# Kernel optimization log

Hardware: AMD Instinct MI355X
Metric: run time of the kernel (lower is better)

Reference implementation:

```python
import jax, jax.numpy as jnp
import numpy as np

N, M, D = 16384, 2048, 512


def setup_inputs() -> dict:
    key = jax.random.key(0)
    k1, k2 = jax.random.split(key)
    x = jax.random.normal(k1, (N, D), dtype=jnp.float32)
    centers = jax.random.normal(k2, (M, D), dtype=jnp.float32)
    log_sigmas = jnp.zeros((M,), dtype=jnp.float32)
    return {"x": x, "centers": centers, "log_sigmas": log_sigmas}


def reference(x, centers, log_sigmas):
    x_sq = jnp.sum(x * x, axis=1, keepdims=True)          # [N, 1]
    c_sq = jnp.sum(centers * centers, axis=1)             # [M]
    cross = jnp.einsum("nd,md->nm", x, centers)           # [N, M] GEMM
    d = x_sq + c_sq[None, :] - 2.0 * cross                # [N, M]
    sigmas = jnp.exp(log_sigmas)                          # [M]
    return jnp.exp(-d / (2.0 * sigmas[None, :] ** 2))     # [N, M]
```

## Files before the change

kernel.cpp:

```cpp
#include <hip/hip_runtime.h>
#include <hip/hip_bf16.h>
#include <stdint.h>

#define N_ROWS 16384
#define M_COLS 2048
#define D_DIM  512

typedef __attribute__((ext_vector_type(4))) float f32x4;
typedef __attribute__((ext_vector_type(2))) int   i32x2;
typedef long i64;

#define AS1 __attribute__((address_space(1)))
#define AS3 __attribute__((address_space(3)))

__global__ __launch_bounds__(256) void conv_all(const float* __restrict__ x,
                                                const float* __restrict__ cen,
                                                const float* __restrict__ ls,
                                                unsigned char* __restrict__ xb,
                                                unsigned char* __restrict__ cb,
                                                float* __restrict__ xsq,
                                                float* __restrict__ csq,
                                                float* __restrict__ nsc) {
  const int gr   = blockIdx.x * 4 + (threadIdx.x >> 6);
  const int lane = threadIdx.x & 63;
  const float* src;
  unsigned char* dst;
  float* sq;
  int row;
  bool is_c = (gr >= N_ROWS);
  if (is_c) { row = gr - N_ROWS; src = cen; dst = cb; sq = csq; }
  else      { row = gr;          src = x;   dst = xb; sq = xsq; }

  const float* s = src + (size_t)row * D_DIM + lane * 8;
  f32x4 v0 = *(const f32x4*)s;
  f32x4 v1 = *(const f32x4*)(s + 4);
  float acc = v0.x*v0.x + v0.y*v0.y + v0.z*v0.z + v0.w*v0.w
            + v1.x*v1.x + v1.y*v1.y + v1.z*v1.z + v1.w*v1.w;
  i32x2 o;
  int w0 = __builtin_amdgcn_cvt_pk_fp8_f32(v0.x, v0.y, 0, false);
  w0     = __builtin_amdgcn_cvt_pk_fp8_f32(v0.z, v0.w, w0, true);
  int w1 = __builtin_amdgcn_cvt_pk_fp8_f32(v1.x, v1.y, 0, false);
  w1     = __builtin_amdgcn_cvt_pk_fp8_f32(v1.z, v1.w, w1, true);
  o[0] = w0; o[1] = w1;
  *(i32x2*)(dst + (size_t)row * D_DIM + lane * 8) = o;
  #pragma unroll
  for (int off = 32; off > 0; off >>= 1) acc += __shfl_down(acc, off, 64);
  if (lane == 0) sq[row] = acc;
  if (is_c && lane == 1) nsc[row] = -0.5f * expf(-2.0f * ls[row]);
}

static __device__ __forceinline__ void gl2lds16(const unsigned char* g, unsigned char* l) {
  __builtin_amdgcn_global_load_lds((const AS1 uint32_t*)g, (AS3 uint32_t*)l, 16, 0, 0);
}

__global__ __launch_bounds__(256) void gemm_rbf(const unsigned char* __restrict__ A8,
                                                const unsigned char* __restrict__ B8,
                                                const float* __restrict__ xsq,
                                                const float* __restrict__ csq,
                                                const float* __restrict__ nscale,
                                                float* __restrict__ out) {
  __shared__ unsigned char As[128 * 128];
  __shared__ unsigned char Bs[128 * 128];

  const int t    = threadIdx.x;
  const int lane = t & 63;
  const int w    = t >> 6;
  const int wr   = w >> 1, wc = w & 1;
  const int rowBase = blockIdx.y * 128;
  const int colBase = blockIdx.x * 128;

  const int lrow = t >> 3;
  const int lkc  = ((t & 7) ^ ((t >> 3) & 7)) * 16;

  const unsigned char* aG = A8 + (size_t)(rowBase + lrow) * D_DIM + lkc;
  const unsigned char* bG = B8 + (size_t)(colBase + lrow) * D_DIM + lkc;
  unsigned char* aL = &As[t * 16];
  unsigned char* bL = &Bs[t * 16];

  f32x4 acc[4][4];
  #pragma unroll
  for (int i = 0; i < 4; ++i)
    #pragma unroll
    for (int j = 0; j < 4; ++j)
      #pragma unroll
      for (int r = 0; r < 4; ++r) acc[i][j][r] = 0.0f;

  const int fr  = lane & 15;
  const int q16 = lane >> 4;
  const int sw  = fr & 7;
  const int sub = (q16 & 1) * 8;

  for (int kt = 0; kt < D_DIM; kt += 128) {
    __syncthreads();
    #pragma unroll
    for (int q = 0; q < 4; ++q) {
      gl2lds16(aG + kt + (size_t)(q * 32) * D_DIM, aL + q * 4096);
      gl2lds16(bG + kt + (size_t)(q * 32) * D_DIM, bL + q * 4096);
    }
    __syncthreads();

    #pragma unroll
    for (int ks = 0; ks < 4; ++ks) {
      const int pc = ((ks * 2 + (q16 >> 1)) ^ sw) * 16 + sub;
      i64 af[4], bfr[4];
      #pragma unroll
      for (int i = 0; i < 4; ++i)
        af[i] = *(const i64*)&As[(wr * 64 + i * 16 + fr) * 128 + pc];
      #pragma unroll
      for (int j = 0; j < 4; ++j)
        bfr[j] = *(const i64*)&Bs[(wc * 64 + j * 16 + fr) * 128 + pc];

      #pragma unroll
      for (int i = 0; i < 4; ++i)
        #pragma unroll
        for (int j = 0; j < 4; ++j)
          acc[i][j] = __builtin_amdgcn_mfma_f32_16x16x32_fp8_fp8(af[i], bfr[j], acc[i][j], 0, 0, 0);
    }
  }

  const int rq = q16 * 4;
  float xs[4][4];
  #pragma unroll
  for (int i = 0; i < 4; ++i)
    #pragma unroll
    for (int r = 0; r < 4; ++r)
      xs[i][r] = xsq[rowBase + wr * 64 + i * 16 + rq + r];

  #pragma unroll
  for (int j = 0; j < 4; ++j) {
    const int c    = colBase + wc * 64 + j * 16 + fr;
    const float cs  = csq[c];
    const float nsc = nscale[c];
    #pragma unroll
    for (int i = 0; i < 4; ++i) {
      const int r0 = rowBase + wr * 64 + i * 16 + rq;
      #pragma unroll
      for (int r = 0; r < 4; ++r) {
        const float dv = xs[i][r] + cs - 2.0f * acc[i][j][r];
        out[(size_t)(r0 + r) * M_COLS + c] = __expf(dv * nsc);
      }
    }
  }
}

__global__ __launch_bounds__(256) void rbf_fallback(const float* __restrict__ x,
                                                    const float* __restrict__ cen,
                                                    const float* __restrict__ ls,
                                                    float* __restrict__ out) {
  __shared__ float xr[D_DIM];
  const int n = blockIdx.y;
  const int m = blockIdx.x * 256 + threadIdx.x;
  for (int d = threadIdx.x; d < D_DIM; d += 256) xr[d] = x[(size_t)n * D_DIM + d];
  __syncthreads();
  const float* cp = cen + (size_t)m * D_DIM;
  float acc = 0.f;
  for (int d = 0; d < D_DIM; d += 4) {
    f32x4 cv = *(const f32x4*)(cp + d);
    float d0 = xr[d + 0] - cv.x;
    float d1 = xr[d + 1] - cv.y;
    float d2 = xr[d + 2] - cv.z;
    float d3 = xr[d + 3] - cv.w;
    acc += d0 * d0 + d1 * d1 + d2 * d2 + d3 * d3;
  }
  const float nsc = -0.5f * expf(-2.0f * ls[m]);
  out[(size_t)n * M_COLS + m] = __expf(acc * nsc);
}

extern "C" void kernel_launch(void* const* d_in, const int* in_sizes, int n_in,
                              void* d_out, int out_size, void* d_ws, size_t ws_size,
                              hipStream_t stream) {
  const float* x   = (const float*)d_in[0];
  const float* cen = (const float*)d_in[1];
  const float* ls  = (const float*)d_in[2];
  float* out = (float*)d_out;

  const size_t need = (size_t)N_ROWS * D_DIM
                    + (size_t)M_COLS * D_DIM
                    + (size_t)N_ROWS * 4
                    + (size_t)M_COLS * 4
                    + (size_t)M_COLS * 4;

  if (ws_size >= need) {
    char* p = (char*)d_ws;
    unsigned char* xb = (unsigned char*)p; p += (size_t)N_ROWS * D_DIM;
    unsigned char* cb = (unsigned char*)p; p += (size_t)M_COLS * D_DIM;
    float* xsq   = (float*)p; p += (size_t)N_ROWS * 4;
    float* csq   = (float*)p; p += (size_t)M_COLS * 4;
    float* nsc   = (float*)p;

    conv_all<<<(N_ROWS + M_COLS) / 4, 256, 0, stream>>>(x, cen, ls, xb, cb, xsq, csq, nsc);
    dim3 grid(M_COLS / 128, N_ROWS / 128);
    gemm_rbf<<<grid, 256, 0, stream>>>(xb, cb, xsq, csq, nsc, out);
  } else {
    dim3 grid(M_COLS / 256, N_ROWS);
    rbf_fallback<<<grid, 256, 0, stream>>>(x, cen, ls, out);
  }
}
```

Measured before the change: 177.2 us.

## Load GEMM fragments directly from global memory into registers with prefetch

Drops the LDS staging and both barriers in the fp8 GEMM. Each lane now loads its MFMA operand fragments straight from global memory as 8-byte loads, double-buffered in registers with one k-step of prefetch. This removes shared-memory traffic and block synchronisation. In exchange, each wave re-reads operands from global/L2 with no cross-wave sharing, and the 8-byte strided loads are poorly coalesced, which likely raises memory traffic.

```diff
diff --git a/kernel.cpp b/kernel.cpp
--- a/kernel.cpp
+++ b/kernel.cpp
@@ -9,9 +9,6 @@
 typedef __attribute__((ext_vector_type(4))) float f32x4;
 typedef __attribute__((ext_vector_type(2))) int   i32x2;
 typedef long i64;
-
-#define AS1 __attribute__((address_space(1)))
-#define AS3 __attribute__((address_space(3)))
 
 __global__ __launch_bounds__(256) void conv_all(const float* __restrict__ x,
                                                 const float* __restrict__ cen,
@@ -49,19 +46,12 @@
   if (is_c && lane == 1) nsc[row] = -0.5f * expf(-2.0f * ls[row]);
 }
 
-static __device__ __forceinline__ void gl2lds16(const unsigned char* g, unsigned char* l) {
-  __builtin_amdgcn_global_load_lds((const AS1 uint32_t*)g, (AS3 uint32_t*)l, 16, 0, 0);
-}
-
 __global__ __launch_bounds__(256) void gemm_rbf(const unsigned char* __restrict__ A8,
                                                 const unsigned char* __restrict__ B8,
                                                 const float* __restrict__ xsq,
                                                 const float* __restrict__ csq,
                                                 const float* __restrict__ nscale,
                                                 float* __restrict__ out) {
-  __shared__ unsigned char As[128 * 128];
-  __shared__ unsigned char Bs[128 * 128];
-
   const int t    = threadIdx.x;
   const int lane = t & 63;
   const int w    = t >> 6;
@@ -69,13 +59,11 @@
   const int rowBase = blockIdx.y * 128;
   const int colBase = blockIdx.x * 128;
 
-  const int lrow = t >> 3;
-  const int lkc  = ((t & 7) ^ ((t >> 3) & 7)) * 16;
+  const int fr  = lane & 15;
+  const int q16 = lane >> 4;
 
-  const unsigned char* aG = A8 + (size_t)(rowBase + lrow) * D_DIM + lkc;
-  const unsigned char* bG = B8 + (size_t)(colBase + lrow) * D_DIM + lkc;
-  unsigned char* aL = &As[t * 16];
-  unsigned char* bL = &Bs[t * 16];
+  const unsigned char* aBase = A8 + (size_t)(rowBase + wr * 64 + fr) * D_DIM + q16 * 8;
+  const unsigned char* bBase = B8 + (size_t)(colBase + wc * 64 + fr) * D_DIM + q16 * 8;
 
   f32x4 acc[4][4];
   #pragma unroll
@@ -85,37 +73,30 @@
       #pragma unroll
       for (int r = 0; r < 4; ++r) acc[i][j][r] = 0.0f;
 
-  const int fr  = lane & 15;
-  const int q16 = lane >> 4;
-  const int sw  = fr & 7;
-  const int sub = (q16 & 1) * 8;
+  i64 aCur[4], bCur[4], aNxt[4], bNxt[4];
+  #pragma unroll
+  for (int i = 0; i < 4; ++i) {
+    aCur[i] = *(const i64*)(aBase + (size_t)(i * 16) * D_DIM);
+    bCur[i] = *(const i64*)(bBase + (size_t)(i * 16) * D_DIM);
+  }
 
-  for (int kt = 0; kt < D_DIM; kt += 128) {
-    __syncthreads();
+  #pragma unroll
+  for (int ks = 0; ks < 16; ++ks) {
+    if (ks < 15) {
+      const int ko = (ks + 1) * 32;
+      #pragma unroll
+      for (int i = 0; i < 4; ++i) {
+        aNxt[i] = *(const i64*)(aBase + (size_t)(i * 16) * D_DIM + ko);
+        bNxt[i] = *(const i64*)(bBase + (size_t)(i * 16) * D_DIM + ko);
+      }
+    }
     #pragma unroll
-    for (int q = 0; q < 4; ++q) {
-      gl2lds16(aG + kt + (size_t)(q * 32) * D_DIM, aL + q * 4096);
-      gl2lds16(bG + kt + (size_t)(q * 32) * D_DIM, bL + q * 4096);
-    }
-    __syncthreads();
-
-    #pragma unroll
-    for (int ks = 0; ks < 4; ++ks) {
-      const int pc = ((ks * 2 + (q16 >> 1)) ^ sw) * 16 + sub;
-      i64 af[4], bfr[4];
-      #pragma unroll
-      for (int i = 0; i < 4; ++i)
-        af[i] = *(const i64*)&As[(wr * 64 + i * 16 + fr) * 128 + pc];
+    for (int i = 0; i < 4; ++i)
       #pragma unroll
       for (int j = 0; j < 4; ++j)
-        bfr[j] = *(const i64*)&Bs[(wc * 64 + j * 16 + fr) * 128 + pc];
-
-      #pragma unroll
-      for (int i = 0; i < 4; ++i)
-        #pragma unroll
-        for (int j = 0; j < 4; ++j)
-          acc[i][j] = __builtin_amdgcn_mfma_f32_16x16x32_fp8_fp8(af[i], bfr[j], acc[i][j], 0, 0, 0);
-    }
+        acc[i][j] = __builtin_amdgcn_mfma_f32_16x16x32_fp8_fp8(aCur[i], bCur[j], acc[i][j], 0, 0, 0);
+    #pragma unroll
+    for (int i = 0; i < 4; ++i) { aCur[i] = aNxt[i]; bCur[i] = bNxt[i]; }
   }
 
   const int rq = q16 * 4;
```

Measured after the change: 263.6 us. +48.7%, slower.

## Double-buffer LDS tiles with K-step 64 to overlap loads and MFMA

Applied to the files above, without the earlier changes.

Splits the K loop into eight 64-wide steps and ping-pongs between two LDS buffers per operand. The global-to-LDS load for the next step is issued right after the barrier, before the MFMAs on the current step, and there is now one barrier per step instead of two. The row mapping and XOR swizzle are reworked for the 64-byte row width to keep LDS reads conflict-free. Total LDS stays the same, but there are more loop iterations and correctness relies on the barrier draining the outstanding async loads.

```diff
diff --git a/kernel.cpp b/kernel.cpp
--- a/kernel.cpp
+++ b/kernel.cpp
@@ -59,8 +59,8 @@
                                                 const float* __restrict__ csq,
                                                 const float* __restrict__ nscale,
                                                 float* __restrict__ out) {
-  __shared__ unsigned char As[128 * 128];
-  __shared__ unsigned char Bs[128 * 128];
+  __shared__ unsigned char As[2][8192];
+  __shared__ unsigned char Bs[2][8192];
 
   const int t    = threadIdx.x;
   const int lane = t & 63;
@@ -69,13 +69,19 @@
   const int rowBase = blockIdx.y * 128;
   const int colBase = blockIdx.x * 128;
 
-  const int lrow = t >> 3;
-  const int lkc  = ((t & 7) ^ ((t >> 3) & 7)) * 16;
-
-  const unsigned char* aG = A8 + (size_t)(rowBase + lrow) * D_DIM + lkc;
-  const unsigned char* bG = B8 + (size_t)(colBase + lrow) * D_DIM + lkc;
-  unsigned char* aL = &As[t * 16];
-  unsigned char* bL = &Bs[t * 16];
+  const unsigned char* aSrc[2];
+  const unsigned char* bSrc[2];
+  #pragma unroll
+  for (int q = 0; q < 2; ++q) {
+    const int s  = q * 256 + t;
+    const int L  = s >> 3;
+    const int p  = s & 7;
+    const int sr = p >> 2;
+    const int c  = (p & 3) ^ (L & 3);
+    const int R  = 2 * L + sr;
+    aSrc[q] = A8 + (size_t)(rowBase + R) * D_DIM + c * 16;
+    bSrc[q] = B8 + (size_t)(colBase + R) * D_DIM + c * 16;
+  }
 
   f32x4 acc[4][4];
   #pragma unroll
@@ -87,28 +93,40 @@
 
   const int fr  = lane & 15;
   const int q16 = lane >> 4;
-  const int sw  = fr & 7;
+  const int key = (fr >> 1) & 3;
   const int sub = (q16 & 1) * 8;
-
-  for (int kt = 0; kt < D_DIM; kt += 128) {
+  const int laneRow = (fr >> 1) * 128 + (fr & 1) * 64;
+
+  #pragma unroll
+  for (int q = 0; q < 2; ++q) {
+    gl2lds16(aSrc[q], &As[0][(q * 256 + t) * 16]);
+    gl2lds16(bSrc[q], &Bs[0][(q * 256 + t) * 16]);
+  }
+
+  for (int kt = 0; kt < 8; ++kt) {
     __syncthreads();
-    #pragma unroll
-    for (int q = 0; q < 4; ++q) {
-      gl2lds16(aG + kt + (size_t)(q * 32) * D_DIM, aL + q * 4096);
-      gl2lds16(bG + kt + (size_t)(q * 32) * D_DIM, bL + q * 4096);
+    if (kt < 7) {
+      const int nb = (kt + 1) & 1;
+      const int ko = (kt + 1) * 64;
+      #pragma unroll
+      for (int q = 0; q < 2; ++q) {
+        gl2lds16(aSrc[q] + ko, &As[nb][(q * 256 + t) * 16]);
+        gl2lds16(bSrc[q] + ko, &Bs[nb][(q * 256 + t) * 16]);
+      }
     }
-    __syncthreads();
-
-    #pragma unroll
-    for (int ks = 0; ks < 4; ++ks) {
-      const int pc = ((ks * 2 + (q16 >> 1)) ^ sw) * 16 + sub;
+    const unsigned char* aBuf = As[kt & 1] + wr * 4096 + laneRow;
+    const unsigned char* bBuf = Bs[kt & 1] + wc * 4096 + laneRow;
+
+    #pragma unroll
+    for (int ks = 0; ks < 2; ++ks) {
+      const int ph = ((ks * 2 + (q16 >> 1)) ^ key) * 16 + sub;
       i64 af[4], bfr[4];
       #pragma unroll
       for (int i = 0; i < 4; ++i)
-        af[i] = *(const i64*)&As[(wr * 64 + i * 16 + fr) * 128 + pc];
+        af[i] = *(const i64*)(aBuf + i * 1024 + ph);
       #pragma unroll
       for (int j = 0; j < 4; ++j)
-        bfr[j] = *(const i64*)&Bs[(wc * 64 + j * 16 + fr) * 128 + pc];
+        bfr[j] = *(const i64*)(bBuf + j * 1024 + ph);
 
       #pragma unroll
       for (int i = 0; i < 4; ++i)
```

After: 181.1 us. 2.2% more time.
